# Performance work log

Hardware: AMD Instinct MI355X
Metric: run time of the kernel (lower is better)

Reference implementation:

```python
import jax, jax.numpy as jnp
import numpy as np

SN, H, W, BN = 4, 128, 128, 65536


def _perspective(fov_deg=60.0, near=0.1, far=100.0):
    f = 1.0 / np.tan(np.deg2rad(fov_deg) / 2.0)
    p = np.zeros((4, 4), np.float32)
    p[0, 0] = f
    p[1, 1] = f
    p[2, 2] = (far + near) / (near - far)
    p[2, 3] = 2.0 * far * near / (near - far)
    p[3, 2] = -1.0
    return p


def setup_inputs() -> dict:
    key = jax.random.key(0)
    ks = jax.random.split(key, 7)
    depth = jax.random.uniform(ks[0], (1, SN, 1, H, W), jnp.float32)
    normal = jax.random.normal(ks[1], (1, SN, 3, H, W), jnp.float32)
    indices = jax.random.randint(ks[2], (BN,), 0, SN, jnp.int32)
    proj = jnp.asarray(_perspective()[None])  # (1,4,4)
    x = jax.random.randint(ks[3], (BN,), 0, W, jnp.int32)
    y = jax.random.randint(ks[4], (BN,), 0, H, jnp.int32)
    d = jax.random.normal(ks[5], (BN, 3), jnp.float32)
    depth_start = jax.random.uniform(ks[6], (BN,), jnp.float32, minval=0.2, maxval=0.8)
    return dict(depth=depth, normal=normal, indices=indices, proj=proj,
                x=x, y=y, d=d, depth_start=depth_start)


def _transform(pos, mat):
    # pos: (bn,3), mat: (4,4) -> homogeneous transform + perspective divide
    pos4 = jnp.concatenate([pos, jnp.ones((pos.shape[0], 1), pos.dtype)], axis=1)
    out = pos4 @ mat.T
    return out[:, :3] / out[:, 3:4]


def _march_next(cur_pos, ray_dir, cur_x, cur_y, h, w, step_x, step_y):
    next_bx = (cur_x + step_x).astype(cur_pos.dtype) / w
    next_by = (cur_y + step_y).astype(cur_pos.dtype) / h
    ncb = jnp.stack([next_bx, 1.0 - next_by], axis=1)          # (bn,2)
    step_ratio = (ncb - cur_pos[:, :2]) / ray_dir[:, :2]       # (bn,2)
    take_y = step_ratio[:, 0] > step_ratio[:, 1]
    dx = jnp.where(take_y, 0, step_x)
    dy = jnp.where(take_y, step_y, 0)
    new_pos = cur_pos + ray_dir * jnp.min(step_ratio, axis=1, keepdims=True)
    return new_pos, dx, dy


def _ssrt(depth, normal, indices, proj, x, y, d, depth_start):
    h, w = depth.shape[2], depth.shape[3]
    bn = x.shape[0]
    unproj = jnp.linalg.inv(proj)
    uv = jnp.stack([(x.astype(jnp.float32) + 0.5) / w,
                    1.0 - (y.astype(jnp.float32) + 0.5) / h], axis=1) * 2.0 - 1.0
    ds = depth_start * 2.0 - 1.0
    proj_pos = jnp.stack([uv[:, 0], uv[:, 1], ds], axis=1)     # (bn,3) NDC
    view_pos = _transform(proj_pos, unproj)
    d_proj = _transform(view_pos + d * 0.001, proj) - proj_pos # projected ray dir
    cur_pos = (proj_pos + 1.0) * 0.5                           # [0,1]^3 screen space
    step_x = jnp.where(d_proj[:, 0] >= 0, 1, -1).astype(x.dtype)
    step_y = jnp.where(d_proj[:, 1] >= 0, -1, 1).astype(y.dtype)
    cur_pos, dx, dy = _march_next(cur_pos, d_proj, x, y, h, w, step_x, step_y)
    cur_x = x + dx
    cur_y = y + dy
    mask = jnp.zeros((bn,), bool)
    results = jnp.zeros((bn, 2), x.dtype)
    dz = jnp.zeros((bn, 1), jnp.float32)

    def cond(state):
        p, _, _, m, _, _ = state
        within = (p[:, 0] >= 0) & (p[:, 0] <= 1) & (p[:, 1] >= 0) & (p[:, 1] <= 1) & (p[:, 2] > 0) & (p[:, 2] < 1)
        return jnp.any(within) & (~jnp.all(m))

    def body(state):
        pos, cx, cy, m, res, dzv = state
        within = (cx >= 0) & (cx < w) & (cy >= 0) & (cy < h)
        xs = jnp.clip(cx, 0, w - 1)
        ys = jnp.clip(cy, 0, h - 1)
        z = depth[indices, 0, ys, xs]                  # (bn,) depth-buffer gather
        nrm = normal[indices, :, ys, xs]               # (bn,3) normal gather
        pz = pos[:, 2]
        hit = within & (pz >= z) & (jnp.sum(d * nrm, axis=1) <= 0) & (~m)
        m = m | hit
        res = jnp.where(hit[:, None], jnp.stack([cx, cy], axis=-1), res)
        dzv = jnp.where(hit[:, None], (pz - z)[:, None], dzv)
        pos, ddx, ddy = _march_next(pos, d_proj, cx, cy, h, w, step_x, step_y)
        return (pos, cx + ddx, cy + ddy, m, res, dzv)

    state = jax.lax.while_loop(cond, body, (cur_pos, cur_x, cur_y, mask, results, dz))
    return state[4], state[3], state[5]


def reference(depth, normal, indices, proj, x, y, d, depth_start):
    return _ssrt(depth[0], normal[0], indices, proj[0], x, y, d, depth_start)
```

## Files before the change

### kernel.cpp

```cpp
#include <hip/hip_runtime.h>
#include <math.h>

#pragma clang fp contract(off)

#define BN 65536
#define SN 4
#define HH 128
#define WW 128

typedef float v4f __attribute__((ext_vector_type(4)));
typedef int v4i __attribute__((ext_vector_type(4)));
__device__ v4f __llvm_buffer_load_v4f32(v4i rsrc, int voffset, int soffset,
                                        int aux) __asm("llvm.amdgcn.raw.buffer.load.v4f32");

__device__ __forceinline__ void inv4(const float* P, float U[4][4]) {
#pragma clang fp contract(off)
    float a = P[10];
    float b = P[11];
    float ra = 1.0f / a;
    float l32 = P[14] * ra;
    float t = l32 * b;
    float u33 = 0.0f - t;
    float rf0 = 1.0f / P[0];
    float rf1 = 1.0f / P[5];
    float ru  = 1.0f / u33;
#pragma unroll
    for (int i = 0; i < 4; i++)
#pragma unroll
        for (int j = 0; j < 4; j++) U[i][j] = 0.0f;
    U[0][0] = rf0;
    U[1][1] = rf1;
    float x3c2 = (0.0f - l32) * ru;
    float y2c2 = fmaf(0.0f - b, x3c2, 1.0f);
    U[2][2] = y2c2 * ra;
    U[3][2] = x3c2;
    float x3c3 = ru;
    float y2c3 = 0.0f - (b * x3c3);
    U[2][3] = y2c3 * ra;
    U[3][3] = x3c3;
}

__device__ __forceinline__ void xform(const float M[4][4], float x, float y, float z,
                                      float& ox, float& oy, float& oz) {
#pragma clang fp contract(off)
    float o[4];
#pragma unroll
    for (int i = 0; i < 4; i++) {
        float acc = x * M[i][0];
        acc = acc + y * M[i][1];
        acc = acc + z * M[i][2];
        acc = acc + M[i][3];
        o[i] = acc;
    }
    ox = o[0] / o[3];
    oy = o[1] / o[3];
    oz = o[2] / o[3];
}

struct RS {
    float p0, p1, p2, d0, d1, d2;
    float y0, y1;
    float fx, cy1;
    float sxf, syf;
    float da, db, dc, hdz;
    int cx, cy, sx, sy, base, B, hoff, hk;
    bool still, testing, hit;
};

__device__ __forceinline__ void make_ray(RS& S, int r, const float* proj,
                                         const int* idxA, const int* xA, const int* yA,
                                         const float* dA, const float* dsA) {
#pragma clang fp contract(off)
    float P[4][4];
#pragma unroll
    for (int i = 0; i < 16; i++) ((float*)P)[i] = proj[i];
    float U[4][4];
    inv4(proj, U);
    int xi = xA[r], yi = yA[r];
    float t0 = ((float)xi + 0.5f) / 128.0f;
    float t1 = 1.0f - ((float)yi + 0.5f) / 128.0f;
    float ux = t0 * 2.0f - 1.0f;
    float uy = t1 * 2.0f - 1.0f;
    float ds = dsA[r] * 2.0f - 1.0f;
    float vx, vy, vz;
    xform(U, ux, uy, ds, vx, vy, vz);
    float ex = vx + dA[3 * r + 0] * 0.001f;
    float ey = vy + dA[3 * r + 1] * 0.001f;
    float ez = vz + dA[3 * r + 2] * 0.001f;
    float qx, qy, qz;
    xform(P, ex, ey, ez, qx, qy, qz);
    S.d0 = qx - ux;
    S.d1 = qy - uy;
    S.d2 = qz - ds;
    S.p0 = (ux + 1.0f) * 0.5f;
    S.p1 = (uy + 1.0f) * 0.5f;
    S.p2 = (ds + 1.0f) * 0.5f;
    S.sx = (S.d0 >= 0.0f) ? 1 : -1;
    S.sy = (S.d1 >= 0.0f) ? -1 : 1;
    S.cx = xi;
    S.cy = yi;
    {
        float nbx = (float)(S.cx + S.sx) / 128.0f;
        float nby = (float)(S.cy + S.sy) / 128.0f;
        float c1 = 1.0f - nby;
        float s0 = (nbx - S.p0) / S.d0;
        float s1 = (c1 - S.p1) / S.d1;
        bool ty = s0 > s1;
        float t = ty ? s1 : s0;
        if (s1 != s1) t = s1;
        S.p0 = S.p0 + S.d0 * t;
        S.p1 = S.p1 + S.d1 * t;
        S.p2 = S.p2 + S.d2 * t;
        if (ty) S.cy += S.sy; else S.cx += S.sx;
    }
    S.y0 = 1.0f / S.d0;
    S.y1 = 1.0f / S.d1;
    S.fx  = (float)(S.cx + S.sx) / 128.0f;
    S.cy1 = 1.0f - (float)(S.cy + S.sy) / 128.0f;
    S.sxf = (float)S.sx * 0.0078125f;
    S.syf = (float)S.sy * 0.0078125f;
    S.da = dA[3 * r + 0]; S.db = dA[3 * r + 1]; S.dc = dA[3 * r + 2];
    S.base = idxA[r] * (HH * WW);
    S.B = 0; S.hoff = 0; S.hk = 0; S.hdz = 0.0f;
    S.still = true; S.testing = true; S.hit = false;
}

__global__ __launch_bounds__(256) void k_pack(const float* __restrict__ depth,
                                              const float* __restrict__ normal,
                                              float4* __restrict__ tab, int* ws) {
    int t = blockIdx.x * 256 + threadIdx.x;
    if (t == 0) ws[0] = 0;
    int s = t >> 14;
    int c = t & 16383;
    float4 v;
    v.x = depth[t];
    v.y = normal[s * 3 * HH * WW + c];
    v.z = normal[s * 3 * HH * WW + HH * WW + c];
    v.w = normal[s * 3 * HH * WW + 2 * HH * WW + c];
    tab[t] = v;
}

__global__ void k_zero(int* ws) { ws[0] = 0; }

template <bool PACKED>
__global__ __launch_bounds__(256, 1) void k_march8(const float* __restrict__ depth,
                                                   const float* __restrict__ normal,
                                                   const float4* __restrict__ tab,
                                                   const int* idxA, const float* proj,
                                                   const int* xA, const int* yA,
                                                   const float* dA, const float* dsA,
                                                   float* out, int* ws) {
#pragma clang fp contract(off)
    int r = blockIdx.x * 256 + threadIdx.x;
    RS S;
    make_ray(S, r, proj, idxA, xA, yA, dA, dsA);
    const float* dep = depth + S.base;
    const float* nrm = normal + 3 * S.base;

    v4i rsrc;
    {
        unsigned long long p = (unsigned long long)(const void*)tab;
        rsrc.x = (int)(p & 0xFFFFFFFFull);
        rsrc.y = (int)(p >> 32);
        rsrc.z = SN * HH * WW * 16;
        rsrc.w = 0x00020000;
    }

#define DECL_SLOT(u) \
    float z##u = 0.0f, a##u = 0.0f, b##u = 0.0f, c##u = 0.0f, q##u = 0.0f; \
    int o##u = 0; bool v##u = false;
    DECL_SLOT(0) DECL_SLOT(1) DECL_SLOT(2) DECL_SLOT(3)
    DECL_SLOT(4) DECL_SLOT(5) DECL_SLOT(6) DECL_SLOT(7)
#undef DECL_SLOT

#define CONSUME(u, kcons) { \
        float t0 = S.da * a##u; \
        float t1 = S.db * b##u; \
        float t2 = S.dc * c##u; \
        float dotv = (t0 + t1) + t2; \
        bool hc = v##u && (q##u >= z##u) && (dotv <= 0.0f) && !S.hit; \
        S.hit = S.hit || hc; \
        S.hoff = hc ? o##u : S.hoff; \
        S.hk   = hc ? (kcons) : S.hk; \
        float dzn = q##u - z##u; \
        S.hdz  = hc ? dzn : S.hdz; \
        v##u = false; }

#define BOXCHK(inow) { \
        bool ib = (S.p0 >= 0.0f) && (S.p0 <= 1.0f) && \
                  (S.p1 >= 0.0f) && (S.p1 <= 1.0f) && \
                  (S.p2 > 0.0f) && (S.p2 < 1.0f); \
        S.still = S.still && ib; \
        S.B = S.still ? ((inow) + 1) : S.B; }

#define MARCH {  \
        float x0 = S.fx - S.p0; \
        float x1 = S.cy1 - S.p1; \
        float q0a = x0 * S.y0; \
        float rra = fmaf(-S.d0, q0a, x0); \
        float s0v = fmaf(rra, S.y0, q0a); \
        float q0b = x1 * S.y1; \
        float rrb = fmaf(-S.d1, q0b, x1); \
        float s1v = fmaf(rrb, S.y1, q0b); \
        bool ty = s0v > s1v; \
        float t = ty ? s1v : s0v; \
        t = (s1v != s1v) ? s1v : t; \
        float m0 = S.d0 * t; S.p0 = S.p0 + m0; \
        float m1 = S.d1 * t; S.p1 = S.p1 + m1; \
        float m2 = S.d2 * t; S.p2 = S.p2 + m2; \
        S.cx  += ty ? 0 : S.sx; \
        S.cy  += ty ? S.sy : 0; \
        S.fx  += ty ? 0.0f : S.sxf; \
        S.cy1 -= ty ? S.syf : 0.0f; }

#define STEP(u, inow) { \
        CONSUME(u, (inow) - 8) \
        BOXCHK(inow) \
        { bool inpix = ((unsigned)S.cx < (unsigned)WW) && ((unsigned)S.cy < (unsigned)HH); \
          bool dead = (S.d2 <= 0.0f) && (S.p2 < 0.0f);    \
          S.testing = S.testing && inpix && !S.hit && !dead; \
          int off = S.cy * WW + S.cx; \
          v##u = S.testing; o##u = off; q##u = S.p2; \
          if (PACKED) { \
              int voff = S.testing ? ((S.base + off) << 4) : 0x40000000; \
              v4f vv = __llvm_buffer_load_v4f32(rsrc, voff, 0, 0); \
              z##u = vv.x; a##u = vv.y; b##u = vv.z; c##u = vv.w; \
          } else if (S.testing) { \
              z##u = dep[off]; \
              a##u = nrm[off]; \
              b##u = nrm[HH * WW + off]; \
              c##u = nrm[2 * HH * WW + off]; \
          } } \
        MARCH \
        __builtin_amdgcn_sched_barrier(0); }

    int i = 0;
    while (i < 4096) {
        STEP(0, i)     STEP(1, i + 1) STEP(2, i + 2) STEP(3, i + 3)
        STEP(4, i + 4) STEP(5, i + 5) STEP(6, i + 6) STEP(7, i + 7)
        i += 8;
        if (!__any(S.testing)) break;
    }
    CONSUME(0, i - 8) CONSUME(1, i - 7) CONSUME(2, i - 6) CONSUME(3, i - 5)
    CONSUME(4, i - 4) CONSUME(5, i - 3) CONSUME(6, i - 2) CONSUME(7, i - 1)

    while (i < 4096 && __any(S.still)) {
#pragma unroll
        for (int u = 0; u < 8; ++u) {
            BOXCHK(i + u)
            MARCH
        }
        i += 8;
    }
#undef STEP
#undef MARCH
#undef BOXCHK
#undef CONSUME

    int pk = S.hit ? (S.hoff | (1 << 14)) : 0;
    out[2 * r]      = (float)pk;
    out[2 * r + 1]  = (float)S.hk;
    out[3 * BN + r] = S.hdz;

    int Bm = S.B;
    for (int o = 32; o; o >>= 1) {
        int v = __shfl_down(Bm, o, 64);
        Bm = Bm > v ? Bm : v;
    }
    if ((threadIdx.x & 63) == 0) atomicMax(ws, Bm);
}

__global__ __launch_bounds__(256) void k_final(float* out, const int* ws) {
    int r = blockIdx.x * 256 + threadIdx.x;
    int N = ws[0];
    int pk = (int)out[2 * r];
    int k  = (int)out[2 * r + 1];
    float dzv = out[3 * BN + r];
    bool hit = (pk >> 14) & 1;
    bool ok = hit && (k < N);
    int rx = pk & 127, ry = (pk >> 7) & 127;
    out[2 * r]      = ok ? (float)rx : 0.0f;
    out[2 * r + 1]  = ok ? (float)ry : 0.0f;
    out[2 * BN + r] = ok ? 1.0f : 0.0f;
    out[3 * BN + r] = ok ? dzv : 0.0f;
}

extern "C" void kernel_launch(void* const* d_in, const int* in_sizes, int n_in,
                              void* d_out, int out_size, void* d_ws, size_t ws_size,
                              hipStream_t stream) {
    const float* depth = (const float*)d_in[0];
    const float* normal = (const float*)d_in[1];
    const int* indices = (const int*)d_in[2];
    const float* proj = (const float*)d_in[3];
    const int* x = (const int*)d_in[4];
    const int* y = (const int*)d_in[5];
    const float* d = (const float*)d_in[6];
    const float* ds = (const float*)d_in[7];
    float* out = (float*)d_out;
    int* ws = (int*)d_ws;

    const size_t tab_off = 64;
    const size_t need = tab_off + (size_t)SN * HH * WW * 16;
    float4* tab = (float4*)((char*)d_ws + tab_off);

    if (ws_size >= need) {
        k_pack<<<(SN * HH * WW) / 256, 256, 0, stream>>>(depth, normal, tab, ws);
        k_march8<true><<<BN / 256, 256, 0, stream>>>(depth, normal, tab, indices,
                                                     proj, x, y, d, ds, out, ws);
    } else {
        k_zero<<<1, 1, 0, stream>>>(ws);
        k_march8<false><<<BN / 256, 256, 0, stream>>>(depth, normal, tab, indices,
                                                      proj, x, y, d, ds, out, ws);
    }
    k_final<<<BN / 256, 256, 0, stream>>>(out, ws);
}
```

Baseline: 43.67 us.

## Split march kernel into separate hit-search and bounding-box kernels

The fused marching kernel, which interleaved the depth/normal gather hit test with the global box-exit iteration count, becomes two kernels. k_hit marches only until each ray hits or leaves the pixel grid. k_box runs the cheap arithmetic-only march (without integer cell updates) to compute the max iteration count. This shortens the live state and register pressure of each loop and drops the sched_barrier, but it recomputes ray setup and march arithmetic twice and adds a kernel launch.

```diff
diff --git a/kernel.cpp b/kernel.cpp
--- a/kernel.cpp
+++ b/kernel.cpp
@@ -125,75 +125,7 @@
     S.still = true; S.testing = true; S.hit = false;
 }
 
-__global__ __launch_bounds__(256) void k_pack(const float* __restrict__ depth,
-                                              const float* __restrict__ normal,
-                                              float4* __restrict__ tab, int* ws) {
-    int t = blockIdx.x * 256 + threadIdx.x;
-    if (t == 0) ws[0] = 0;
-    int s = t >> 14;
-    int c = t & 16383;
-    float4 v;
-    v.x = depth[t];
-    v.y = normal[s * 3 * HH * WW + c];
-    v.z = normal[s * 3 * HH * WW + HH * WW + c];
-    v.w = normal[s * 3 * HH * WW + 2 * HH * WW + c];
-    tab[t] = v;
-}
-
-__global__ void k_zero(int* ws) { ws[0] = 0; }
-
-template <bool PACKED>
-__global__ __launch_bounds__(256, 1) void k_march8(const float* __restrict__ depth,
-                                                   const float* __restrict__ normal,
-                                                   const float4* __restrict__ tab,
-                                                   const int* idxA, const float* proj,
-                                                   const int* xA, const int* yA,
-                                                   const float* dA, const float* dsA,
-                                                   float* out, int* ws) {
-#pragma clang fp contract(off)
-    int r = blockIdx.x * 256 + threadIdx.x;
-    RS S;
-    make_ray(S, r, proj, idxA, xA, yA, dA, dsA);
-    const float* dep = depth + S.base;
-    const float* nrm = normal + 3 * S.base;
-
-    v4i rsrc;
-    {
-        unsigned long long p = (unsigned long long)(const void*)tab;
-        rsrc.x = (int)(p & 0xFFFFFFFFull);
-        rsrc.y = (int)(p >> 32);
-        rsrc.z = SN * HH * WW * 16;
-        rsrc.w = 0x00020000;
-    }
-
-#define DECL_SLOT(u) \
-    float z##u = 0.0f, a##u = 0.0f, b##u = 0.0f, c##u = 0.0f, q##u = 0.0f; \
-    int o##u = 0; bool v##u = false;
-    DECL_SLOT(0) DECL_SLOT(1) DECL_SLOT(2) DECL_SLOT(3)
-    DECL_SLOT(4) DECL_SLOT(5) DECL_SLOT(6) DECL_SLOT(7)
-#undef DECL_SLOT
-
-#define CONSUME(u, kcons) { \
-        float t0 = S.da * a##u; \
-        float t1 = S.db * b##u; \
-        float t2 = S.dc * c##u; \
-        float dotv = (t0 + t1) + t2; \
-        bool hc = v##u && (q##u >= z##u) && (dotv <= 0.0f) && !S.hit; \
-        S.hit = S.hit || hc; \
-        S.hoff = hc ? o##u : S.hoff; \
-        S.hk   = hc ? (kcons) : S.hk; \
-        float dzn = q##u - z##u; \
-        S.hdz  = hc ? dzn : S.hdz; \
-        v##u = false; }
-
-#define BOXCHK(inow) { \
-        bool ib = (S.p0 >= 0.0f) && (S.p0 <= 1.0f) && \
-                  (S.p1 >= 0.0f) && (S.p1 <= 1.0f) && \
-                  (S.p2 > 0.0f) && (S.p2 < 1.0f); \
-        S.still = S.still && ib; \
-        S.B = S.still ? ((inow) + 1) : S.B; }
-
-#define MARCH {  \
+#define MARCH { \
         float x0 = S.fx - S.p0; \
         float x1 = S.cy1 - S.p1; \
         float q0a = x0 * S.y0; \
@@ -213,9 +145,119 @@
         S.fx  += ty ? 0.0f : S.sxf; \
         S.cy1 -= ty ? S.syf : 0.0f; }
 
+#define MARCH_NB { \
+        float x0 = S.fx - S.p0; \
+        float x1 = S.cy1 - S.p1; \
+        float q0a = x0 * S.y0; \
+        float rra = fmaf(-S.d0, q0a, x0); \
+        float s0v = fmaf(rra, S.y0, q0a); \
+        float q0b = x1 * S.y1; \
+        float rrb = fmaf(-S.d1, q0b, x1); \
+        float s1v = fmaf(rrb, S.y1, q0b); \
+        bool ty = s0v > s1v; \
+        float t = ty ? s1v : s0v; \
+        t = (s1v != s1v) ? s1v : t; \
+        float m0 = S.d0 * t; S.p0 = S.p0 + m0; \
+        float m1 = S.d1 * t; S.p1 = S.p1 + m1; \
+        float m2 = S.d2 * t; S.p2 = S.p2 + m2; \
+        S.fx  += ty ? 0.0f : S.sxf; \
+        S.cy1 -= ty ? S.syf : 0.0f; }
+
+#define BOXCHK(inow) { \
+        bool ib = (S.p0 >= 0.0f) && (S.p0 <= 1.0f) && \
+                  (S.p1 >= 0.0f) && (S.p1 <= 1.0f) && \
+                  (S.p2 > 0.0f) && (S.p2 < 1.0f); \
+        S.still = S.still && ib; \
+        S.B = S.still ? ((inow) + 1) : S.B; }
+
+__global__ __launch_bounds__(256) void k_pack(const float* __restrict__ depth,
+                                              const float* __restrict__ normal,
+                                              float4* __restrict__ tab, int* ws) {
+    int t = blockIdx.x * 256 + threadIdx.x;
+    if (t == 0) ws[0] = 0;
+    int s = t >> 14;
+    int c = t & 16383;
+    float4 v;
+    v.x = depth[t];
+    v.y = normal[s * 3 * HH * WW + c];
+    v.z = normal[s * 3 * HH * WW + HH * WW + c];
+    v.w = normal[s * 3 * HH * WW + 2 * HH * WW + c];
+    tab[t] = v;
+}
+
+__global__ void k_zero(int* ws) { ws[0] = 0; }
+
+__global__ __launch_bounds__(256, 1) void k_box(const int* idxA, const float* proj,
+                                                const int* xA, const int* yA,
+                                                const float* dA, const float* dsA,
+                                                int* ws) {
+#pragma clang fp contract(off)
+    int r = blockIdx.x * 256 + threadIdx.x;
+    RS S;
+    make_ray(S, r, proj, idxA, xA, yA, dA, dsA);
+    int i = 0;
+    while (i < 4096 && __any(S.still)) {
+#pragma unroll
+        for (int u = 0; u < 8; ++u) {
+            BOXCHK(i + u)
+            MARCH_NB
+        }
+        i += 8;
+    }
+    int Bm = S.B;
+    for (int o = 32; o; o >>= 1) {
+        int v = __shfl_down(Bm, o, 64);
+        Bm = Bm > v ? Bm : v;
+    }
+    if ((threadIdx.x & 63) == 0) atomicMax(ws, Bm);
+}
+
+template <bool PACKED>
+__global__ __launch_bounds__(256, 1) void k_hit(const float* __restrict__ depth,
+                                                const float* __restrict__ normal,
+                                                const float4* __restrict__ tab,
+                                                const int* idxA, const float* proj,
+                                                const int* xA, const int* yA,
+                                                const float* dA, const float* dsA,
+                                                float* out) {
+#pragma clang fp contract(off)
+    int r = blockIdx.x * 256 + threadIdx.x;
+    RS S;
+    make_ray(S, r, proj, idxA, xA, yA, dA, dsA);
+    const float* dep = depth + S.base;
+    const float* nrm = normal + 3 * S.base;
+
+    v4i rsrc;
+    {
+        unsigned long long p = (unsigned long long)(const void*)tab;
+        rsrc.x = (int)(p & 0xFFFFFFFFull);
+        rsrc.y = (int)(p >> 32);
+        rsrc.z = SN * HH * WW * 16;
+        rsrc.w = 0x00020000;
+    }
+
+#define DECL_SLOT(u) \
+    float z##u = 0.0f, a##u = 0.0f, b##u = 0.0f, c##u = 0.0f, q##u = 0.0f; \
+    int o##u = 0; bool v##u = false;
+    DECL_SLOT(0) DECL_SLOT(1) DECL_SLOT(2) DECL_SLOT(3)
+    DECL_SLOT(4) DECL_SLOT(5) DECL_SLOT(6) DECL_SLOT(7)
+#undef DECL_SLOT
+
+#define CONSUME(u, kcons) { \
+        float t0 = S.da * a##u; \
+        float t1 = S.db * b##u; \
+        float t2 = S.dc * c##u; \
+        float dotv = (t0 + t1) + t2; \
+        bool hc = v##u && (q##u >= z##u) && (dotv <= 0.0f) && !S.hit; \
+        S.hit = S.hit || hc; \
+        S.hoff = hc ? o##u : S.hoff; \
+        S.hk   = hc ? (kcons) : S.hk; \
+        float dzn = q##u - z##u; \
+        S.hdz  = hc ? dzn : S.hdz; \
+        v##u = false; }
+
 #define STEP(u, inow) { \
         CONSUME(u, (inow) - 8) \
-        BOXCHK(inow) \
         { bool inpix = ((unsigned)S.cx < (unsigned)WW) && ((unsigned)S.cy < (unsigned)HH); \
           bool dead = (S.d2 <= 0.0f) && (S.p2 < 0.0f);    \
           S.testing = S.testing && inpix && !S.hit && !dead; \
@@ -231,8 +273,7 @@
               b##u = nrm[HH * WW + off]; \
               c##u = nrm[2 * HH * WW + off]; \
           } } \
-        MARCH \
-        __builtin_amdgcn_sched_barrier(0); }
+        MARCH }
 
     int i = 0;
     while (i < 4096) {
@@ -243,31 +284,13 @@
     }
     CONSUME(0, i - 8) CONSUME(1, i - 7) CONSUME(2, i - 6) CONSUME(3, i - 5)
     CONSUME(4, i - 4) CONSUME(5, i - 3) CONSUME(6, i - 2) CONSUME(7, i - 1)
-
-    while (i < 4096 && __any(S.still)) {
-#pragma unroll
-        for (int u = 0; u < 8; ++u) {
-            BOXCHK(i + u)
-            MARCH
-        }
-        i += 8;
-    }
 #undef STEP
-#undef MARCH
-#undef BOXCHK
 #undef CONSUME
 
     int pk = S.hit ? (S.hoff | (1 << 14)) : 0;
     out[2 * r]      = (float)pk;
     out[2 * r + 1]  = (float)S.hk;
     out[3 * BN + r] = S.hdz;
-
-    int Bm = S.B;
-    for (int o = 32; o; o >>= 1) {
-        int v = __shfl_down(Bm, o, 64);
-        Bm = Bm > v ? Bm : v;
-    }
-    if ((threadIdx.x & 63) == 0) atomicMax(ws, Bm);
 }
 
 __global__ __launch_bounds__(256) void k_final(float* out, const int* ws) {
@@ -305,12 +328,14 @@
 
     if (ws_size >= need) {
         k_pack<<<(SN * HH * WW) / 256, 256, 0, stream>>>(depth, normal, tab, ws);
-        k_march8<true><<<BN / 256, 256, 0, stream>>>(depth, normal, tab, indices,
-                                                     proj, x, y, d, ds, out, ws);
+        k_hit<true><<<BN / 256, 256, 0, stream>>>(depth, normal, tab, indices,
+                                                  proj, x, y, d, ds, out);
+        k_box<<<BN / 256, 256, 0, stream>>>(indices, proj, x, y, d, ds, ws);
     } else {
         k_zero<<<1, 1, 0, stream>>>(ws);
-        k_march8<false><<<BN / 256, 256, 0, stream>>>(depth, normal, tab, indices,
-                                                      proj, x, y, d, ds, out, ws);
+        k_hit<false><<<BN / 256, 256, 0, stream>>>(depth, normal, tab, indices,
+                                                   proj, x, y, d, ds, out);
+        k_box<<<BN / 256, 256, 0, stream>>>(indices, proj, x, y, d, ds, ws);
     }
     k_final<<<BN / 256, 256, 0, stream>>>(out, ws);
 }
```

Result: slower. 54.44 us (+24.7%).

## Split each ray's march across two threads covering steps 0-127 and 128-255

Applied to the files above, without the earlier changes.

The packed-table march kernel now assigns two threads per ray. The first thread tests steps 0..127, and the second re-marches its first 128 steps without loads and then tests steps 128..255. Results are merged through shared memory, with the lower-half hit taking priority. This aims to cut the serial dependency chain per ray and double thread-level parallelism. It also caps marching at 256 steps instead of 4096, which changes results for rays needing more steps, and it removes the sched_barrier.

```diff
diff --git a/kernel.cpp b/kernel.cpp
--- a/kernel.cpp
+++ b/kernel.cpp
@@ -125,75 +125,7 @@
     S.still = true; S.testing = true; S.hit = false;
 }
 
-__global__ __launch_bounds__(256) void k_pack(const float* __restrict__ depth,
-                                              const float* __restrict__ normal,
-                                              float4* __restrict__ tab, int* ws) {
-    int t = blockIdx.x * 256 + threadIdx.x;
-    if (t == 0) ws[0] = 0;
-    int s = t >> 14;
-    int c = t & 16383;
-    float4 v;
-    v.x = depth[t];
-    v.y = normal[s * 3 * HH * WW + c];
-    v.z = normal[s * 3 * HH * WW + HH * WW + c];
-    v.w = normal[s * 3 * HH * WW + 2 * HH * WW + c];
-    tab[t] = v;
-}
-
-__global__ void k_zero(int* ws) { ws[0] = 0; }
-
-template <bool PACKED>
-__global__ __launch_bounds__(256, 1) void k_march8(const float* __restrict__ depth,
-                                                   const float* __restrict__ normal,
-                                                   const float4* __restrict__ tab,
-                                                   const int* idxA, const float* proj,
-                                                   const int* xA, const int* yA,
-                                                   const float* dA, const float* dsA,
-                                                   float* out, int* ws) {
-#pragma clang fp contract(off)
-    int r = blockIdx.x * 256 + threadIdx.x;
-    RS S;
-    make_ray(S, r, proj, idxA, xA, yA, dA, dsA);
-    const float* dep = depth + S.base;
-    const float* nrm = normal + 3 * S.base;
-
-    v4i rsrc;
-    {
-        unsigned long long p = (unsigned long long)(const void*)tab;
-        rsrc.x = (int)(p & 0xFFFFFFFFull);
-        rsrc.y = (int)(p >> 32);
-        rsrc.z = SN * HH * WW * 16;
-        rsrc.w = 0x00020000;
-    }
-
-#define DECL_SLOT(u) \
-    float z##u = 0.0f, a##u = 0.0f, b##u = 0.0f, c##u = 0.0f, q##u = 0.0f; \
-    int o##u = 0; bool v##u = false;
-    DECL_SLOT(0) DECL_SLOT(1) DECL_SLOT(2) DECL_SLOT(3)
-    DECL_SLOT(4) DECL_SLOT(5) DECL_SLOT(6) DECL_SLOT(7)
-#undef DECL_SLOT
-
-#define CONSUME(u, kcons) { \
-        float t0 = S.da * a##u; \
-        float t1 = S.db * b##u; \
-        float t2 = S.dc * c##u; \
-        float dotv = (t0 + t1) + t2; \
-        bool hc = v##u && (q##u >= z##u) && (dotv <= 0.0f) && !S.hit; \
-        S.hit = S.hit || hc; \
-        S.hoff = hc ? o##u : S.hoff; \
-        S.hk   = hc ? (kcons) : S.hk; \
-        float dzn = q##u - z##u; \
-        S.hdz  = hc ? dzn : S.hdz; \
-        v##u = false; }
-
-#define BOXCHK(inow) { \
-        bool ib = (S.p0 >= 0.0f) && (S.p0 <= 1.0f) && \
-                  (S.p1 >= 0.0f) && (S.p1 <= 1.0f) && \
-                  (S.p2 > 0.0f) && (S.p2 < 1.0f); \
-        S.still = S.still && ib; \
-        S.B = S.still ? ((inow) + 1) : S.B; }
-
-#define MARCH {  \
+#define MARCH { \
         float x0 = S.fx - S.p0; \
         float x1 = S.cy1 - S.p1; \
         float q0a = x0 * S.y0; \
@@ -213,55 +145,209 @@
         S.fx  += ty ? 0.0f : S.sxf; \
         S.cy1 -= ty ? S.syf : 0.0f; }
 
-#define STEP(u, inow) { \
+#define BOXCHK(inow, bse) { \
+        bool ib = (S.p0 >= 0.0f) && (S.p0 <= 1.0f) && \
+                  (S.p1 >= 0.0f) && (S.p1 <= 1.0f) && \
+                  (S.p2 > 0.0f) && (S.p2 < 1.0f); \
+        S.still = S.still && ib; \
+        S.B = S.still ? ((inow) + 1 - (bse)) : S.B; }
+
+#define CONSUME(u, kcons) { \
+        float t0 = S.da * a##u; \
+        float t1 = S.db * b##u; \
+        float t2 = S.dc * c##u; \
+        float dotv = (t0 + t1) + t2; \
+        bool hc = v##u && (q##u >= z##u) && (dotv <= 0.0f) && !S.hit; \
+        S.hit = S.hit || hc; \
+        S.hoff = hc ? o##u : S.hoff; \
+        S.hk   = hc ? (kcons) : S.hk; \
+        float dzn = q##u - z##u; \
+        S.hdz  = hc ? dzn : S.hdz; \
+        v##u = false; }
+
+#define STEP(u, inow, bse) { \
         CONSUME(u, (inow) - 8) \
-        BOXCHK(inow) \
+        BOXCHK(inow, bse) \
         { bool inpix = ((unsigned)S.cx < (unsigned)WW) && ((unsigned)S.cy < (unsigned)HH); \
           bool dead = (S.d2 <= 0.0f) && (S.p2 < 0.0f);    \
           S.testing = S.testing && inpix && !S.hit && !dead; \
           int off = S.cy * WW + S.cx; \
           v##u = S.testing; o##u = off; q##u = S.p2; \
-          if (PACKED) { \
-              int voff = S.testing ? ((S.base + off) << 4) : 0x40000000; \
-              v4f vv = __llvm_buffer_load_v4f32(rsrc, voff, 0, 0); \
-              z##u = vv.x; a##u = vv.y; b##u = vv.z; c##u = vv.w; \
-          } else if (S.testing) { \
+          int voff = S.testing ? ((S.base + off) << 4) : 0x40000000; \
+          v4f vv = __llvm_buffer_load_v4f32(rsrc, voff, 0, 0); \
+          z##u = vv.x; a##u = vv.y; b##u = vv.z; c##u = vv.w; } \
+        MARCH }
+
+#define DECL_SLOTS \
+    float z0=0,a0=0,b0=0,c0=0,q0=0; int o0=0; bool v0=false; \
+    float z1=0,a1=0,b1=0,c1=0,q1=0; int o1=0; bool v1=false; \
+    float z2=0,a2=0,b2=0,c2=0,q2=0; int o2=0; bool v2=false; \
+    float z3=0,a3=0,b3=0,c3=0,q3=0; int o3=0; bool v3=false; \
+    float z4=0,a4=0,b4=0,c4=0,q4=0; int o4=0; bool v4=false; \
+    float z5=0,a5=0,b5=0,c5=0,q5=0; int o5=0; bool v5=false; \
+    float z6=0,a6=0,b6=0,c6=0,q6=0; int o6=0; bool v6=false; \
+    float z7=0,a7=0,b7=0,c7=0,q7=0; int o7=0; bool v7=false;
+
+__global__ __launch_bounds__(256) void k_pack(const float* __restrict__ depth,
+                                              const float* __restrict__ normal,
+                                              float4* __restrict__ tab, int* ws) {
+    int t = blockIdx.x * 256 + threadIdx.x;
+    if (t == 0) ws[0] = 0;
+    int s = t >> 14;
+    int c = t & 16383;
+    float4 v;
+    v.x = depth[t];
+    v.y = normal[s * 3 * HH * WW + c];
+    v.z = normal[s * 3 * HH * WW + HH * WW + c];
+    v.w = normal[s * 3 * HH * WW + 2 * HH * WW + c];
+    tab[t] = v;
+}
+
+__global__ void k_zero(int* ws) { ws[0] = 0; }
+
+__global__ __launch_bounds__(256, 1) void k_march_s(const float4* __restrict__ tab,
+                                                    const int* idxA, const float* proj,
+                                                    const int* xA, const int* yA,
+                                                    const float* dA, const float* dsA,
+                                                    float* out, int* ws) {
+#pragma clang fp contract(off)
+    __shared__ int smPk[128];
+    __shared__ int smK[128];
+    __shared__ float smDz[128];
+    __shared__ int smLB[128];
+
+    int tid = threadIdx.x;
+    bool isB = tid >= 128;
+    int r = blockIdx.x * 128 + (tid & 127);
+    RS S;
+    make_ray(S, r, proj, idxA, xA, yA, dA, dsA);
+
+    v4i rsrc;
+    {
+        unsigned long long p = (unsigned long long)(const void*)tab;
+        rsrc.x = (int)(p & 0xFFFFFFFFull);
+        rsrc.y = (int)(p >> 32);
+        rsrc.z = SN * HH * WW * 16;
+        rsrc.w = 0x00020000;
+    }
+
+    DECL_SLOTS
+
+    if (!isB) {
+        int i = 0;
+        while (i < 128 && __any(S.testing)) {
+            STEP(0, i, 0)     STEP(1, i + 1, 0) STEP(2, i + 2, 0) STEP(3, i + 3, 0)
+            STEP(4, i + 4, 0) STEP(5, i + 5, 0) STEP(6, i + 6, 0) STEP(7, i + 7, 0)
+            i += 8;
+        }
+        CONSUME(0, i - 8) CONSUME(1, i - 7) CONSUME(2, i - 6) CONSUME(3, i - 5)
+        CONSUME(4, i - 4) CONSUME(5, i - 3) CONSUME(6, i - 2) CONSUME(7, i - 1)
+        while (i < 128 && __any(S.still)) {
+#pragma unroll
+            for (int u = 0; u < 8; ++u) {
+                BOXCHK(i + u, 0)
+                MARCH
+            }
+            i += 8;
+        }
+    } else {
+        for (int j = 0; j < 16; ++j) {
+#pragma unroll
+            for (int u = 0; u < 8; ++u) MARCH
+        }
+        int i = 128;
+        while (i < 256 && __any(S.testing)) {
+            STEP(0, i, 128)     STEP(1, i + 1, 128) STEP(2, i + 2, 128) STEP(3, i + 3, 128)
+            STEP(4, i + 4, 128) STEP(5, i + 5, 128) STEP(6, i + 6, 128) STEP(7, i + 7, 128)
+            i += 8;
+        }
+        CONSUME(0, i - 8) CONSUME(1, i - 7) CONSUME(2, i - 6) CONSUME(3, i - 5)
+        CONSUME(4, i - 4) CONSUME(5, i - 3) CONSUME(6, i - 2) CONSUME(7, i - 1)
+        while (i < 256 && __any(S.still)) {
+#pragma unroll
+            for (int u = 0; u < 8; ++u) {
+                BOXCHK(i + u, 128)
+                MARCH
+            }
+            i += 8;
+        }
+        int idx = tid - 128;
+        smPk[idx] = S.hit ? (S.hoff | (1 << 14)) : 0;
+        smK[idx]  = S.hk;
+        smDz[idx] = S.hdz;
+        smLB[idx] = S.B;
+    }
+    __syncthreads();
+    if (!isB) {
+        int idx = tid;
+        int pkB = smPk[idx];
+        bool hA = S.hit;
+        bool hB = (pkB >> 14) & 1;
+        int pk  = hA ? (S.hoff | (1 << 14)) : (hB ? pkB : 0);
+        int k   = hA ? S.hk : (hB ? smK[idx] : 0);
+        float dz = hA ? S.hdz : (hB ? smDz[idx] : 0.0f);
+        int Bm = (S.B == 128) ? (128 + smLB[idx]) : S.B;
+        out[2 * r]      = (float)pk;
+        out[2 * r + 1]  = (float)k;
+        out[3 * BN + r] = dz;
+        for (int o = 32; o; o >>= 1) {
+            int v = __shfl_down(Bm, o, 64);
+            Bm = Bm > v ? Bm : v;
+        }
+        if ((tid & 63) == 0) atomicMax(ws, Bm);
+    }
+}
+
+__global__ __launch_bounds__(256, 1) void k_march_mono(const float* __restrict__ depth,
+                                                       const float* __restrict__ normal,
+                                                       const int* idxA, const float* proj,
+                                                       const int* xA, const int* yA,
+                                                       const float* dA, const float* dsA,
+                                                       float* out, int* ws) {
+#pragma clang fp contract(off)
+    int r = blockIdx.x * 256 + threadIdx.x;
+    RS S;
+    make_ray(S, r, proj, idxA, xA, yA, dA, dsA);
+    const float* dep = depth + S.base;
+    const float* nrm = normal + 3 * S.base;
+    DECL_SLOTS
+#define STEPU(u, inow) { \
+        CONSUME(u, (inow) - 8) \
+        BOXCHK(inow, 0) \
+        { bool inpix = ((unsigned)S.cx < (unsigned)WW) && ((unsigned)S.cy < (unsigned)HH); \
+          bool dead = (S.d2 <= 0.0f) && (S.p2 < 0.0f); \
+          S.testing = S.testing && inpix && !S.hit && !dead; \
+          int off = S.cy * WW + S.cx; \
+          v##u = S.testing; o##u = off; q##u = S.p2; \
+          if (S.testing) { \
               z##u = dep[off]; \
               a##u = nrm[off]; \
               b##u = nrm[HH * WW + off]; \
               c##u = nrm[2 * HH * WW + off]; \
           } } \
-        MARCH \
-        __builtin_amdgcn_sched_barrier(0); }
-
+        MARCH }
     int i = 0;
     while (i < 4096) {
-        STEP(0, i)     STEP(1, i + 1) STEP(2, i + 2) STEP(3, i + 3)
-        STEP(4, i + 4) STEP(5, i + 5) STEP(6, i + 6) STEP(7, i + 7)
+        STEPU(0, i)     STEPU(1, i + 1) STEPU(2, i + 2) STEPU(3, i + 3)
+        STEPU(4, i + 4) STEPU(5, i + 5) STEPU(6, i + 6) STEPU(7, i + 7)
         i += 8;
         if (!__any(S.testing)) break;
     }
     CONSUME(0, i - 8) CONSUME(1, i - 7) CONSUME(2, i - 6) CONSUME(3, i - 5)
     CONSUME(4, i - 4) CONSUME(5, i - 3) CONSUME(6, i - 2) CONSUME(7, i - 1)
-
     while (i < 4096 && __any(S.still)) {
 #pragma unroll
         for (int u = 0; u < 8; ++u) {
-            BOXCHK(i + u)
+            BOXCHK(i + u, 0)
             MARCH
         }
         i += 8;
     }
-#undef STEP
-#undef MARCH
-#undef BOXCHK
-#undef CONSUME
-
+#undef STEPU
     int pk = S.hit ? (S.hoff | (1 << 14)) : 0;
     out[2 * r]      = (float)pk;
     out[2 * r + 1]  = (float)S.hk;
     out[3 * BN + r] = S.hdz;
-
     int Bm = S.B;
     for (int o = 32; o; o >>= 1) {
         int v = __shfl_down(Bm, o, 64);
@@ -305,12 +391,11 @@
 
     if (ws_size >= need) {
         k_pack<<<(SN * HH * WW) / 256, 256, 0, stream>>>(depth, normal, tab, ws);
-        k_march8<true><<<BN / 256, 256, 0, stream>>>(depth, normal, tab, indices,
-                                                     proj, x, y, d, ds, out, ws);
+        k_march_s<<<BN / 128, 256, 0, stream>>>(tab, indices, proj, x, y, d, ds, out, ws);
     } else {
         k_zero<<<1, 1, 0, stream>>>(ws);
-        k_march8<false><<<BN / 256, 256, 0, stream>>>(depth, normal, tab, indices,
-                                                      proj, x, y, d, ds, out, ws);
+        k_march_mono<<<BN / 256, 256, 0, stream>>>(depth, normal, indices, proj,
+                                                   x, y, d, ds, out, ws);
     }
     k_final<<<BN / 256, 256, 0, stream>>>(out, ws);
 }
```

After: 42.71 us. -2.2%, faster.

## Prefilter march hits with an LDS-resident truncated depth copy

Applied to the files above, without the earlier changes.

Each block first copies the whole depth buffer into 128KB of LDS as the upper 16 bits of every float. The march loop then tests this truncated depth from LDS, and only issues the packed depth+normal global gather for pixels that could be hits. Because the truncated value never exceeds the true depth, the final exact check stays correct. The work becomes a two-stage software pipeline with a 16-step lag, and the sched_barrier is dropped. In exchange every block repeats a 256KB global read to fill LDS and runs with the large LDS allocation, which caps occupancy.

```diff
diff --git a/kernel.cpp b/kernel.cpp
--- a/kernel.cpp
+++ b/kernel.cpp
@@ -125,75 +125,7 @@
     S.still = true; S.testing = true; S.hit = false;
 }
 
-__global__ __launch_bounds__(256) void k_pack(const float* __restrict__ depth,
-                                              const float* __restrict__ normal,
-                                              float4* __restrict__ tab, int* ws) {
-    int t = blockIdx.x * 256 + threadIdx.x;
-    if (t == 0) ws[0] = 0;
-    int s = t >> 14;
-    int c = t & 16383;
-    float4 v;
-    v.x = depth[t];
-    v.y = normal[s * 3 * HH * WW + c];
-    v.z = normal[s * 3 * HH * WW + HH * WW + c];
-    v.w = normal[s * 3 * HH * WW + 2 * HH * WW + c];
-    tab[t] = v;
-}
-
-__global__ void k_zero(int* ws) { ws[0] = 0; }
-
-template <bool PACKED>
-__global__ __launch_bounds__(256, 1) void k_march8(const float* __restrict__ depth,
-                                                   const float* __restrict__ normal,
-                                                   const float4* __restrict__ tab,
-                                                   const int* idxA, const float* proj,
-                                                   const int* xA, const int* yA,
-                                                   const float* dA, const float* dsA,
-                                                   float* out, int* ws) {
-#pragma clang fp contract(off)
-    int r = blockIdx.x * 256 + threadIdx.x;
-    RS S;
-    make_ray(S, r, proj, idxA, xA, yA, dA, dsA);
-    const float* dep = depth + S.base;
-    const float* nrm = normal + 3 * S.base;
-
-    v4i rsrc;
-    {
-        unsigned long long p = (unsigned long long)(const void*)tab;
-        rsrc.x = (int)(p & 0xFFFFFFFFull);
-        rsrc.y = (int)(p >> 32);
-        rsrc.z = SN * HH * WW * 16;
-        rsrc.w = 0x00020000;
-    }
-
-#define DECL_SLOT(u) \
-    float z##u = 0.0f, a##u = 0.0f, b##u = 0.0f, c##u = 0.0f, q##u = 0.0f; \
-    int o##u = 0; bool v##u = false;
-    DECL_SLOT(0) DECL_SLOT(1) DECL_SLOT(2) DECL_SLOT(3)
-    DECL_SLOT(4) DECL_SLOT(5) DECL_SLOT(6) DECL_SLOT(7)
-#undef DECL_SLOT
-
-#define CONSUME(u, kcons) { \
-        float t0 = S.da * a##u; \
-        float t1 = S.db * b##u; \
-        float t2 = S.dc * c##u; \
-        float dotv = (t0 + t1) + t2; \
-        bool hc = v##u && (q##u >= z##u) && (dotv <= 0.0f) && !S.hit; \
-        S.hit = S.hit || hc; \
-        S.hoff = hc ? o##u : S.hoff; \
-        S.hk   = hc ? (kcons) : S.hk; \
-        float dzn = q##u - z##u; \
-        S.hdz  = hc ? dzn : S.hdz; \
-        v##u = false; }
-
-#define BOXCHK(inow) { \
-        bool ib = (S.p0 >= 0.0f) && (S.p0 <= 1.0f) && \
-                  (S.p1 >= 0.0f) && (S.p1 <= 1.0f) && \
-                  (S.p2 > 0.0f) && (S.p2 < 1.0f); \
-        S.still = S.still && ib; \
-        S.B = S.still ? ((inow) + 1) : S.B; }
-
-#define MARCH {  \
+#define MARCH { \
         float x0 = S.fx - S.p0; \
         float x1 = S.cy1 - S.p1; \
         float q0a = x0 * S.y0; \
@@ -213,26 +145,105 @@
         S.fx  += ty ? 0.0f : S.sxf; \
         S.cy1 -= ty ? S.syf : 0.0f; }
 
+#define BOXCHK(inow) { \
+        bool ib = (S.p0 >= 0.0f) && (S.p0 <= 1.0f) && \
+                  (S.p1 >= 0.0f) && (S.p1 <= 1.0f) && \
+                  (S.p2 > 0.0f) && (S.p2 < 1.0f); \
+        S.still = S.still && ib; \
+        S.B = S.still ? ((inow) + 1) : S.B; }
+
+__global__ __launch_bounds__(256) void k_pack(const float* __restrict__ depth,
+                                              const float* __restrict__ normal,
+                                              float4* __restrict__ tab, int* ws) {
+    int t = blockIdx.x * 256 + threadIdx.x;
+    if (t == 0) ws[0] = 0;
+    int s = t >> 14;
+    int c = t & 16383;
+    float4 v;
+    v.x = depth[t];
+    v.y = normal[s * 3 * HH * WW + c];
+    v.z = normal[s * 3 * HH * WW + HH * WW + c];
+    v.w = normal[s * 3 * HH * WW + 2 * HH * WW + c];
+    tab[t] = v;
+}
+
+__global__ void k_zero(int* ws) { ws[0] = 0; }
+
+__global__ __launch_bounds__(256, 1) void k_marchZ(const float* __restrict__ depth,
+                                                   const float4* __restrict__ tab,
+                                                   const int* idxA, const float* proj,
+                                                   const int* xA, const int* yA,
+                                                   const float* dA, const float* dsA,
+                                                   float* out, int* ws) {
+#pragma clang fp contract(off)
+    extern __shared__ unsigned short zs[];
+    for (int j = threadIdx.x; j < (SN * HH * WW) / 4; j += 256) {
+        float4 dv = ((const float4*)depth)[j];
+        ushort4 o;
+        o.x = (unsigned short)(__float_as_uint(dv.x) >> 16);
+        o.y = (unsigned short)(__float_as_uint(dv.y) >> 16);
+        o.z = (unsigned short)(__float_as_uint(dv.z) >> 16);
+        o.w = (unsigned short)(__float_as_uint(dv.w) >> 16);
+        ((ushort4*)zs)[j] = o;
+    }
+    __syncthreads();
+
+    int r = blockIdx.x * 256 + threadIdx.x;
+    RS S;
+    make_ray(S, r, proj, idxA, xA, yA, dA, dsA);
+
+    v4i rsrc;
+    {
+        unsigned long long p = (unsigned long long)(const void*)tab;
+        rsrc.x = (int)(p & 0xFFFFFFFFull);
+        rsrc.y = (int)(p >> 32);
+        rsrc.z = SN * HH * WW * 16;
+        rsrc.w = 0x00020000;
+    }
+
+#define DECL_Z(u) int zr##u = 0, zo##u = 0; float zq##u = 0.0f; bool zv##u = false;
+#define DECL_N(u) v4f nld##u = {0,0,0,0}; int no##u = 0; float nq##u = 0.0f; bool nv##u = false;
+    DECL_Z(0) DECL_Z(1) DECL_Z(2) DECL_Z(3) DECL_Z(4) DECL_Z(5) DECL_Z(6) DECL_Z(7)
+    DECL_N(0) DECL_N(1) DECL_N(2) DECL_N(3) DECL_N(4) DECL_N(5) DECL_N(6) DECL_N(7)
+#undef DECL_Z
+#undef DECL_N
+
+#define CONSUME_N(u, kcons) { \
+        float t0 = S.da * nld##u.y; \
+        float t1 = S.db * nld##u.z; \
+        float t2 = S.dc * nld##u.w; \
+        float dotv = (t0 + t1) + t2; \
+        bool hc = nv##u && (nq##u >= nld##u.x) && (dotv <= 0.0f) && !S.hit; \
+        S.hit = S.hit || hc; \
+        S.hoff = hc ? no##u : S.hoff; \
+        S.hk   = hc ? (kcons) : S.hk; \
+        float dzn = nq##u - nld##u.x; \
+        S.hdz  = hc ? dzn : S.hdz; \
+        nv##u = false; }
+
+#define CONSUME_Z(u) { \
+        float zf = __uint_as_float(((unsigned)zr##u) << 16); \
+        bool cand = zv##u && (zq##u >= zf); \
+        int voff = cand ? ((S.base + zo##u) << 4) : 0x40000000; \
+        v4f vv = __llvm_buffer_load_v4f32(rsrc, voff, 0, 0); \
+        nld##u = vv; nv##u = cand; nq##u = zq##u; no##u = zo##u; \
+        zv##u = false; }
+
+#define ISSUE_Z(u, inow) { \
+        bool inpix = ((unsigned)S.cx < (unsigned)WW) && ((unsigned)S.cy < (unsigned)HH); \
+        bool dead = (S.d2 <= 0.0f) && (S.p2 < 0.0f); \
+        S.testing = S.testing && inpix && !S.hit && !dead; \
+        int off = S.cy * WW + S.cx; \
+        int zaddr = S.testing ? (S.base + off) : 0; \
+        zr##u = zs[zaddr]; \
+        zv##u = S.testing; zo##u = off; zq##u = S.p2; }
+
 #define STEP(u, inow) { \
-        CONSUME(u, (inow) - 8) \
+        CONSUME_N(u, (inow) - 16) \
+        CONSUME_Z(u) \
         BOXCHK(inow) \
-        { bool inpix = ((unsigned)S.cx < (unsigned)WW) && ((unsigned)S.cy < (unsigned)HH); \
-          bool dead = (S.d2 <= 0.0f) && (S.p2 < 0.0f);    \
-          S.testing = S.testing && inpix && !S.hit && !dead; \
-          int off = S.cy * WW + S.cx; \
-          v##u = S.testing; o##u = off; q##u = S.p2; \
-          if (PACKED) { \
-              int voff = S.testing ? ((S.base + off) << 4) : 0x40000000; \
-              v4f vv = __llvm_buffer_load_v4f32(rsrc, voff, 0, 0); \
-              z##u = vv.x; a##u = vv.y; b##u = vv.z; c##u = vv.w; \
-          } else if (S.testing) { \
-              z##u = dep[off]; \
-              a##u = nrm[off]; \
-              b##u = nrm[HH * WW + off]; \
-              c##u = nrm[2 * HH * WW + off]; \
-          } } \
-        MARCH \
-        __builtin_amdgcn_sched_barrier(0); }
+        ISSUE_Z(u, inow) \
+        MARCH }
 
     int i = 0;
     while (i < 4096) {
@@ -241,8 +252,12 @@
         i += 8;
         if (!__any(S.testing)) break;
     }
-    CONSUME(0, i - 8) CONSUME(1, i - 7) CONSUME(2, i - 6) CONSUME(3, i - 5)
-    CONSUME(4, i - 4) CONSUME(5, i - 3) CONSUME(6, i - 2) CONSUME(7, i - 1)
+    CONSUME_N(0, i - 16) CONSUME_N(1, i - 15) CONSUME_N(2, i - 14) CONSUME_N(3, i - 13)
+    CONSUME_N(4, i - 12) CONSUME_N(5, i - 11) CONSUME_N(6, i - 10) CONSUME_N(7, i - 9)
+    CONSUME_Z(0) CONSUME_Z(1) CONSUME_Z(2) CONSUME_Z(3)
+    CONSUME_Z(4) CONSUME_Z(5) CONSUME_Z(6) CONSUME_Z(7)
+    CONSUME_N(0, i - 8) CONSUME_N(1, i - 7) CONSUME_N(2, i - 6) CONSUME_N(3, i - 5)
+    CONSUME_N(4, i - 4) CONSUME_N(5, i - 3) CONSUME_N(6, i - 2) CONSUME_N(7, i - 1)
 
     while (i < 4096 && __any(S.still)) {
 #pragma unroll
@@ -253,15 +268,91 @@
         i += 8;
     }
 #undef STEP
-#undef MARCH
-#undef BOXCHK
-#undef CONSUME
+#undef ISSUE_Z
+#undef CONSUME_Z
+#undef CONSUME_N
 
     int pk = S.hit ? (S.hoff | (1 << 14)) : 0;
     out[2 * r]      = (float)pk;
     out[2 * r + 1]  = (float)S.hk;
     out[3 * BN + r] = S.hdz;
 
+    int Bm = S.B;
+    for (int o = 32; o; o >>= 1) {
+        int v = __shfl_down(Bm, o, 64);
+        Bm = Bm > v ? Bm : v;
+    }
+    if ((threadIdx.x & 63) == 0) atomicMax(ws, Bm);
+}
+
+__global__ __launch_bounds__(256, 1) void k_march_mono(const float* __restrict__ depth,
+                                                       const float* __restrict__ normal,
+                                                       const int* idxA, const float* proj,
+                                                       const int* xA, const int* yA,
+                                                       const float* dA, const float* dsA,
+                                                       float* out, int* ws) {
+#pragma clang fp contract(off)
+    int r = blockIdx.x * 256 + threadIdx.x;
+    RS S;
+    make_ray(S, r, proj, idxA, xA, yA, dA, dsA);
+    const float* dep = depth + S.base;
+    const float* nrm = normal + 3 * S.base;
+#define DECL_SLOT(u) \
+    float z##u = 0.0f, a##u = 0.0f, b##u = 0.0f, c##u = 0.0f, q##u = 0.0f; \
+    int o##u = 0; bool v##u = false;
+    DECL_SLOT(0) DECL_SLOT(1) DECL_SLOT(2) DECL_SLOT(3)
+    DECL_SLOT(4) DECL_SLOT(5) DECL_SLOT(6) DECL_SLOT(7)
+#undef DECL_SLOT
+#define CONSUME(u, kcons) { \
+        float t0 = S.da * a##u; \
+        float t1 = S.db * b##u; \
+        float t2 = S.dc * c##u; \
+        float dotv = (t0 + t1) + t2; \
+        bool hc = v##u && (q##u >= z##u) && (dotv <= 0.0f) && !S.hit; \
+        S.hit = S.hit || hc; \
+        S.hoff = hc ? o##u : S.hoff; \
+        S.hk   = hc ? (kcons) : S.hk; \
+        float dzn = q##u - z##u; \
+        S.hdz  = hc ? dzn : S.hdz; \
+        v##u = false; }
+#define STEPU(u, inow) { \
+        CONSUME(u, (inow) - 8) \
+        BOXCHK(inow) \
+        { bool inpix = ((unsigned)S.cx < (unsigned)WW) && ((unsigned)S.cy < (unsigned)HH); \
+          bool dead = (S.d2 <= 0.0f) && (S.p2 < 0.0f); \
+          S.testing = S.testing && inpix && !S.hit && !dead; \
+          int off = S.cy * WW + S.cx; \
+          v##u = S.testing; o##u = off; q##u = S.p2; \
+          if (S.testing) { \
+              z##u = dep[off]; \
+              a##u = nrm[off]; \
+              b##u = nrm[HH * WW + off]; \
+              c##u = nrm[2 * HH * WW + off]; \
+          } } \
+        MARCH }
+    int i = 0;
+    while (i < 4096) {
+        STEPU(0, i)     STEPU(1, i + 1) STEPU(2, i + 2) STEPU(3, i + 3)
+        STEPU(4, i + 4) STEPU(5, i + 5) STEPU(6, i + 6) STEPU(7, i + 7)
+        i += 8;
+        if (!__any(S.testing)) break;
+    }
+    CONSUME(0, i - 8) CONSUME(1, i - 7) CONSUME(2, i - 6) CONSUME(3, i - 5)
+    CONSUME(4, i - 4) CONSUME(5, i - 3) CONSUME(6, i - 2) CONSUME(7, i - 1)
+    while (i < 4096 && __any(S.still)) {
+#pragma unroll
+        for (int u = 0; u < 8; ++u) {
+            BOXCHK(i + u)
+            MARCH
+        }
+        i += 8;
+    }
+#undef STEPU
+#undef CONSUME
+    int pk = S.hit ? (S.hoff | (1 << 14)) : 0;
+    out[2 * r]      = (float)pk;
+    out[2 * r + 1]  = (float)S.hk;
+    out[3 * BN + r] = S.hdz;
     int Bm = S.B;
     for (int o = 32; o; o >>= 1) {
         int v = __shfl_down(Bm, o, 64);
@@ -302,15 +393,23 @@
     const size_t tab_off = 64;
     const size_t need = tab_off + (size_t)SN * HH * WW * 16;
     float4* tab = (float4*)((char*)d_ws + tab_off);
+    const int lds_bytes = SN * HH * WW * 2;
+
+    static bool attr_done = false;
+    if (!attr_done) {
+        hipFuncSetAttribute((const void*)k_marchZ,
+                            hipFuncAttributeMaxDynamicSharedMemorySize, lds_bytes);
+        attr_done = true;
+    }
 
     if (ws_size >= need) {
         k_pack<<<(SN * HH * WW) / 256, 256, 0, stream>>>(depth, normal, tab, ws);
-        k_march8<true><<<BN / 256, 256, 0, stream>>>(depth, normal, tab, indices,
-                                                     proj, x, y, d, ds, out, ws);
+        k_marchZ<<<BN / 256, 256, lds_bytes, stream>>>(depth, tab, indices, proj,
+                                                       x, y, d, ds, out, ws);
     } else {
         k_zero<<<1, 1, 0, stream>>>(ws);
-        k_march8<false><<<BN / 256, 256, 0, stream>>>(depth, normal, tab, indices,
-                                                      proj, x, y, d, ds, out, ws);
+        k_march_mono<<<BN / 256, 256, 0, stream>>>(depth, normal, indices, proj,
+                                                   x, y, d, ds, out, ws);
     }
     k_final<<<BN / 256, 256, 0, stream>>>(out, ws);
 }
```

Result: slower. 48.34 us (+10.7%).
